# Optimization experiments

Hardware: AMD Instinct MI355X
Metric: run time of the kernel (lower is better)

The kernel has to match this reference:

```python
import jax, jax.numpy as jnp
import numpy as np

INV_SQRT2 = 0.7071067811865476  # 1/sqrt(2), orthonormal Haar
N_LEVELS = 3


def setup_inputs() -> dict:
    key = jax.random.key(0)
    ks = jax.random.split(key, 5)
    B, S, D = 16, 4096, 512
    x = jax.random.normal(ks[0], (B, S, D), dtype=jnp.float32)
    sizes = [256, 128, 64]  # detail-band sizes for 3-level DWT of 512
    Wd0 = jax.random.normal(ks[1], (sizes[0], sizes[0]), dtype=jnp.float32) * 0.02
    Wd1 = jax.random.normal(ks[2], (sizes[1], sizes[1]), dtype=jnp.float32) * 0.02
    Wd2 = jax.random.normal(ks[3], (sizes[2], sizes[2]), dtype=jnp.float32) * 0.02
    Wa = jax.random.normal(ks[4], (sizes[2], sizes[2]), dtype=jnp.float32) * 0.02
    return {
        'x': x,
        'Wd0': Wd0, 'bd0': jnp.zeros((sizes[0],), jnp.float32),
        'Wd1': Wd1, 'bd1': jnp.zeros((sizes[1],), jnp.float32),
        'Wd2': Wd2, 'bd2': jnp.zeros((sizes[2],), jnp.float32),
        'Wa': Wa, 'ba': jnp.zeros((sizes[2],), jnp.float32),
    }


def reference(x, Wd0, bd0, Wd1, bd1, Wd2, bd2, Wa, ba):
    # Multi-level Haar DWT along the feature axis.
    details = []
    a = x
    for _ in range(N_LEVELS):
        e = a[..., 0::2]
        o = a[..., 1::2]
        details.append((e - o) * INV_SQRT2)  # detail coefficients
        a = (e + o) * INV_SQRT2              # approximation coefficients

    # Per-level small linear transforms (torch Linear: y = x @ W.T + b).
    Wds, bds = [Wd0, Wd1, Wd2], [bd0, bd1, bd2]
    details = [details[i] @ Wds[i].T + bds[i] for i in range(N_LEVELS)]
    a = a @ Wa.T + ba

    # Inverse Haar DWT (orthonormal): even=(a+d)/sqrt2, odd=(a-d)/sqrt2, interleave.
    for i in reversed(range(N_LEVELS)):
        d = details[i]
        e = (a + d) * INV_SQRT2
        o = (a - d) * INV_SQRT2
        a = jnp.stack([e, o], axis=-1).reshape(a.shape[:-1] + (a.shape[-1] * 2,))
    return a
```

## Files before the change

kernel.cpp:

```cpp
#include <hip/hip_runtime.h>
#include <stdint.h>

typedef float  f32x4  __attribute__((ext_vector_type(4)));
typedef short  bf16x8 __attribute__((ext_vector_type(8)));
typedef int    i32x4  __attribute__((ext_vector_type(4)));
typedef unsigned int u32x2 __attribute__((ext_vector_type(2)));

#define C1f 0.70710678118654752f
#define C2f 0.5f
#define C3f 0.35355339059327373f

#define NT 512
#define CH 64
#define RB 1040
#define CHSZ (CH*RB)
#define RPB 256
#define NCHUNK (RPB/CH)
#define NCOLG 4

__device__ __forceinline__ unsigned int f2b(float f) {
    unsigned int u; __builtin_memcpy(&u, &f, 4);
    u += 0x7fffu + ((u >> 16) & 1u);
    return u >> 16;
}
__device__ __forceinline__ unsigned int pack2(float lo, float hi) {
    return f2b(lo) | (f2b(hi) << 16);
}
__device__ __forceinline__ bf16x8 cast8(i32x4 v) {
    bf16x8 r; __builtin_memcpy(&r, &v, 16); return r;
}

__device__ __forceinline__ void lds_barrier() {
    asm volatile("s_waitcnt lgkmcnt(0)" ::: "memory");
    __builtin_amdgcn_s_barrier();
    __builtin_amdgcn_sched_barrier(0);
}
__device__ __forceinline__ void vwait4() {
    asm volatile("s_waitcnt vmcnt(4)" ::: "memory");
    __builtin_amdgcn_sched_barrier(0);
}

__device__ __forceinline__ bf16x8 g_frag(int o, int i0,
        const float* __restrict__ W0, const float* __restrict__ W1,
        const float* __restrict__ W2, const float* __restrict__ Wa)
{
    const float s0o = (o & 1) ? -1.f : 1.f;
    const float s1o = ((o >> 1) & 1) ? -1.f : 1.f;
    const float s2o = ((o >> 2) & 1) ? -1.f : 1.f;
    const float4 w0 = *(const float4*)(W0 + (o >> 1) * 256 + (i0 >> 1));
    const float2 w1 = *(const float2*)(W1 + (o >> 2) * 128 + (i0 >> 2));
    const float  w2 = W2[(o >> 3) * 64 + (i0 >> 3)];
    const float  wa = Wa[(o >> 3) * 64 + (i0 >> 3)];
    const float base = 0.125f * wa;
    const float c2   = 0.125f * s2o * w2;
    const float c1   = 0.25f  * s1o;
    const float c0   = 0.5f   * s0o;
    const float w0a[4] = { w0.x, w0.y, w0.z, w0.w };
    const float w1a[2] = { w1.x, w1.y };
    float g[8];
    #pragma unroll
    for (int e = 0; e < 8; ++e) {
        const float t2 = ((e >> 2) & 1) ? -c2 : c2;
        const float t1 = (((e >> 1) & 1) ? -c1 : c1) * w1a[e >> 2];
        const float t0 = ((e & 1) ? -c0 : c0) * w0a[e >> 1];
        g[e] = base + t2 + t1 + t0;
    }
    i32x4 p = { (int)pack2(g[0],g[1]), (int)pack2(g[2],g[3]),
                (int)pack2(g[4],g[5]), (int)pack2(g[6],g[7]) };
    return cast8(p);
}

__global__ void prep(const float* __restrict__ W0, const float* __restrict__ b0,
                     const float* __restrict__ W1, const float* __restrict__ b1,
                     const float* __restrict__ W2, const float* __restrict__ b2,
                     const float* __restrict__ Wa, const float* __restrict__ ba,
                     unsigned short* __restrict__ ws)
{
    const int gid  = blockIdx.x * 256 + threadIdx.x;
    const int blob = gid >> 6, lane = gid & 63;
    const int otg  = blob >> 4, ks = blob & 15;
    const int o  = otg * 16 + (lane & 15);
    const int i0 = ks * 32 + ((lane >> 4) * 8);
    bf16x8 f = g_frag(o, i0, W0, W1, W2, Wa);
    i32x4 p; __builtin_memcpy(&p, &f, 16);
    *(i32x4*)(ws + blob * 512 + lane * 8) = p;
    if (gid < 512) {
        float* gv = (float*)(ws + 262144);
        const int oo = gid;
        const float s0 = (oo & 1) ? -C1f : C1f;
        const float s1 = ((oo >> 1) & 1) ? -C2f : C2f;
        const float s2 = ((oo >> 2) & 1) ? -C3f : C3f;
        gv[oo] = C3f * ba[oo >> 3] + s2 * b2[oo >> 3] + s1 * b1[oo >> 2] + s0 * b0[oo >> 1];
    }
}

template<int USE_WS>
__global__ __launch_bounds__(NT, 2)
void wavelet_gemm(const float* __restrict__ x,
                  const float* __restrict__ W0, const float* __restrict__ b0,
                  const float* __restrict__ W1, const float* __restrict__ b1,
                  const float* __restrict__ W2, const float* __restrict__ b2,
                  const float* __restrict__ Wa, const float* __restrict__ ba,
                  const unsigned short* __restrict__ wsb,
                  float* __restrict__ out, int nblk)
{
    __shared__ char lds[2 * CHSZ];

    const int tid  = threadIdx.x;
    const int lane = tid & 63;
    const int wave = tid >> 6;

    const int cpx = nblk >> 3;
    const int lbid = ((int)blockIdx.x & 7) * cpx + ((int)blockIdx.x >> 3);
    const int colg = lbid & (NCOLG - 1);
    const long rowblk = (long)(lbid >> 2) * RPB;

    const int otg  = colg * 8 + wave;
    const int col0 = otg * 16;
    const int bc0  = col0 + ((lane >> 4) << 2);

    bf16x8 B[16];
    if (USE_WS) {
        #pragma unroll
        for (int ks = 0; ks < 16; ++ks)
            B[ks] = cast8(*(const i32x4*)(wsb + ((size_t)(otg * 16 + ks) * 512) + lane * 8));
    } else {
        #pragma unroll
        for (int ks = 0; ks < 16; ++ks)
            B[ks] = g_frag(col0 + (lane & 15), ks * 32 + ((lane >> 4) * 8), W0, W1, W2, Wa);
    }
    #pragma unroll
    for (int ks = 0; ks < 16; ++ks) {
        i32x4 t; __builtin_memcpy(&t, &B[ks], 16);
        asm volatile("" : "+v"(t));
        __builtin_memcpy(&B[ks], &t, 16);
    }

    f32x4 gv4;
    if (USE_WS) {
        const float4 g4 = *(const float4*)((const float*)(wsb + 262144) + bc0);
        gv4 = f32x4{ g4.x, g4.y, g4.z, g4.w };
    } else {
        #pragma unroll
        for (int j = 0; j < 4; ++j) {
            const int col = bc0 + j;
            const float s0 = (col & 1) ? -C1f : C1f;
            const float s1 = ((col >> 1) & 1) ? -C2f : C2f;
            const float s2 = ((col >> 2) & 1) ? -C3f : C3f;
            gv4[j] = C3f * ba[col >> 3] + s2 * b2[col >> 3] + s1 * b1[col >> 2] + s0 * b0[col >> 1];
        }
    }

    auto ldx = [&](int c, f32x4* v) {
        const f32x4* xb = (const f32x4*)(x + (rowblk + (long)c * CH) * 512);
        #pragma unroll
        for (int i = 0; i < 16; ++i) v[i] = xb[i * NT + tid];
    };
    auto stx = [&](int c, const f32x4* v) {
        char* base = lds + (c & 1) * CHSZ;
        #pragma unroll
        for (int i = 0; i < 16; ++i) {
            const int f = i * NT + tid;
            const int row = f >> 7, c4 = f & 127;
            u32x2 p = { pack2(v[i][0], v[i][1]), pack2(v[i][2], v[i][3]) };
            *(u32x2*)(base + row * RB + c4 * 8) = p;
        }
    };
    auto compute = [&](int c) {
        const char* base = lds + (c & 1) * CHSZ + (lane & 15) * RB + ((lane >> 4) * 16);
        const long r0 = rowblk + (long)c * CH + (lane & 15);
        #pragma unroll
        for (int m = 0; m < 4; ++m) {
            const char* pa = base + m * 16 * RB;
            f32x4 acc = {};
            #pragma unroll
            for (int ks = 0; ks < 16; ++ks) {
                bf16x8 a = cast8(*(const i32x4*)(pa + ks * 64));
                acc = __builtin_amdgcn_mfma_f32_16x16x32_bf16(B[ks], a, acc, 0, 0, 0);
            }
            *(f32x4*)(out + (r0 + m * 16) * 512 + bc0) = acc + gv4;
        }
    };

    {
        f32x4 v[16];
        ldx(0, v);
        stx(0, v);
    }
    lds_barrier();

    #pragma unroll 1
    for (int c = 0; c < NCHUNK; ++c) {
        f32x4 vn[16];
        if (c + 1 < NCHUNK) {
            ldx(c + 1, vn);
            __builtin_amdgcn_sched_barrier(0);
        }
        compute(c);
        if (c + 1 < NCHUNK) {
            vwait4();
            stx(c + 1, vn);
            lds_barrier();
        }
    }
}

extern "C" void kernel_launch(void* const* d_in, const int* in_sizes, int n_in,
                              void* d_out, int out_size, void* d_ws, size_t ws_size,
                              hipStream_t stream)
{
    const float* x  = (const float*)d_in[0];
    const float* W0 = (const float*)d_in[1];
    const float* b0 = (const float*)d_in[2];
    const float* W1 = (const float*)d_in[3];
    const float* b1 = (const float*)d_in[4];
    const float* W2 = (const float*)d_in[5];
    const float* b2 = (const float*)d_in[6];
    const float* Wa = (const float*)d_in[7];
    const float* ba = (const float*)d_in[8];
    float* out = (float*)d_out;

    const int nrows = in_sizes[0] / 512;
    const int nblk  = (nrows / RPB) * NCOLG;

    if (ws_size >= (size_t)(524288 + 2048)) {
        unsigned short* ws = (unsigned short*)d_ws;
        prep<<<128, 256, 0, stream>>>(W0, b0, W1, b1, W2, b2, Wa, ba, ws);
        wavelet_gemm<1><<<nblk, NT, 0, stream>>>(x, W0, b0, W1, b1, W2, b2, Wa, ba, ws, out, nblk);
    } else {
        wavelet_gemm<0><<<nblk, NT, 0, stream>>>(x, W0, b0, W1, b1, W2, b2, Wa, ba, nullptr, out, nblk);
    }
}
```

Baseline: 88.13 us.

## Give each wave two output column tiles and halve row chunk size

```diff
diff --git a/kernel.cpp b/kernel.cpp
--- a/kernel.cpp
+++ b/kernel.cpp
@@ -11,12 +11,11 @@
 #define C3f 0.35355339059327373f
 
 #define NT 512
-#define CH 64
+#define CH 32
 #define RB 1040
 #define CHSZ (CH*RB)
 #define RPB 256
 #define NCHUNK (RPB/CH)
-#define NCOLG 4
 
 __device__ __forceinline__ unsigned int f2b(float f) {
     unsigned int u; __builtin_memcpy(&u, &f, 4);
@@ -112,54 +111,67 @@
 
     const int cpx = nblk >> 3;
     const int lbid = ((int)blockIdx.x & 7) * cpx + ((int)blockIdx.x >> 3);
-    const int colg = lbid & (NCOLG - 1);
-    const long rowblk = (long)(lbid >> 2) * RPB;
-
-    const int otg  = colg * 8 + wave;
-    const int col0 = otg * 16;
+    const int chalf = lbid & 1;
+    const long rowblk = (long)(lbid >> 1) * RPB;
+
+    const int otg0 = chalf * 16 + wave * 2;
+    const int col0 = otg0 * 16;
     const int bc0  = col0 + ((lane >> 4) << 2);
 
-    bf16x8 B[16];
+    bf16x8 B0[16], B1[16];
     if (USE_WS) {
         #pragma unroll
-        for (int ks = 0; ks < 16; ++ks)
-            B[ks] = cast8(*(const i32x4*)(wsb + ((size_t)(otg * 16 + ks) * 512) + lane * 8));
+        for (int ks = 0; ks < 16; ++ks) {
+            B0[ks] = cast8(*(const i32x4*)(wsb + ((size_t)(otg0 * 16 + ks) * 512) + lane * 8));
+            B1[ks] = cast8(*(const i32x4*)(wsb + ((size_t)((otg0 + 1) * 16 + ks) * 512) + lane * 8));
+        }
     } else {
         #pragma unroll
-        for (int ks = 0; ks < 16; ++ks)
-            B[ks] = g_frag(col0 + (lane & 15), ks * 32 + ((lane >> 4) * 8), W0, W1, W2, Wa);
+        for (int ks = 0; ks < 16; ++ks) {
+            B0[ks] = g_frag(col0 + (lane & 15),      ks * 32 + ((lane >> 4) * 8), W0, W1, W2, Wa);
+            B1[ks] = g_frag(col0 + 16 + (lane & 15), ks * 32 + ((lane >> 4) * 8), W0, W1, W2, Wa);
+        }
     }
     #pragma unroll
     for (int ks = 0; ks < 16; ++ks) {
-        i32x4 t; __builtin_memcpy(&t, &B[ks], 16);
-        asm volatile("" : "+v"(t));
-        __builtin_memcpy(&B[ks], &t, 16);
-    }
-
-    f32x4 gv4;
+        i32x4 t0, t1;
+        __builtin_memcpy(&t0, &B0[ks], 16);
+        __builtin_memcpy(&t1, &B1[ks], 16);
+        asm volatile("" : "+v"(t0), "+v"(t1));
+        __builtin_memcpy(&B0[ks], &t0, 16);
+        __builtin_memcpy(&B1[ks], &t1, 16);
+    }
+
+    f32x4 gv40, gv41;
     if (USE_WS) {
-        const float4 g4 = *(const float4*)((const float*)(wsb + 262144) + bc0);
-        gv4 = f32x4{ g4.x, g4.y, g4.z, g4.w };
+        const float4 g0 = *(const float4*)((const float*)(wsb + 262144) + bc0);
+        const float4 g1 = *(const float4*)((const float*)(wsb + 262144) + bc0 + 16);
+        gv40 = f32x4{ g0.x, g0.y, g0.z, g0.w };
+        gv41 = f32x4{ g1.x, g1.y, g1.z, g1.w };
     } else {
         #pragma unroll
         for (int j = 0; j < 4; ++j) {
-            const int col = bc0 + j;
-            const float s0 = (col & 1) ? -C1f : C1f;
-            const float s1 = ((col >> 1) & 1) ? -C2f : C2f;
-            const float s2 = ((col >> 2) & 1) ? -C3f : C3f;
-            gv4[j] = C3f * ba[col >> 3] + s2 * b2[col >> 3] + s1 * b1[col >> 2] + s0 * b0[col >> 1];
+            #pragma unroll
+            for (int t = 0; t < 2; ++t) {
+                const int col = bc0 + t * 16 + j;
+                const float s0 = (col & 1) ? -C1f : C1f;
+                const float s1 = ((col >> 1) & 1) ? -C2f : C2f;
+                const float s2 = ((col >> 2) & 1) ? -C3f : C3f;
+                const float v = C3f * ba[col >> 3] + s2 * b2[col >> 3] + s1 * b1[col >> 2] + s0 * b0[col >> 1];
+                if (t == 0) gv40[j] = v; else gv41[j] = v;
+            }
         }
     }
 
     auto ldx = [&](int c, f32x4* v) {
         const f32x4* xb = (const f32x4*)(x + (rowblk + (long)c * CH) * 512);
         #pragma unroll
-        for (int i = 0; i < 16; ++i) v[i] = xb[i * NT + tid];
+        for (int i = 0; i < 8; ++i) v[i] = xb[i * NT + tid];
     };
     auto stx = [&](int c, const f32x4* v) {
         char* base = lds + (c & 1) * CHSZ;
         #pragma unroll
-        for (int i = 0; i < 16; ++i) {
+        for (int i = 0; i < 8; ++i) {
             const int f = i * NT + tid;
             const int row = f >> 7, c4 = f & 127;
             u32x2 p = { pack2(v[i][0], v[i][1]), pack2(v[i][2], v[i][3]) };
@@ -170,20 +182,23 @@
         const char* base = lds + (c & 1) * CHSZ + (lane & 15) * RB + ((lane >> 4) * 16);
         const long r0 = rowblk + (long)c * CH + (lane & 15);
         #pragma unroll
-        for (int m = 0; m < 4; ++m) {
+        for (int m = 0; m < 2; ++m) {
             const char* pa = base + m * 16 * RB;
-            f32x4 acc = {};
+            f32x4 acc0 = {}, acc1 = {};
             #pragma unroll
             for (int ks = 0; ks < 16; ++ks) {
                 bf16x8 a = cast8(*(const i32x4*)(pa + ks * 64));
-                acc = __builtin_amdgcn_mfma_f32_16x16x32_bf16(B[ks], a, acc, 0, 0, 0);
+                acc0 = __builtin_amdgcn_mfma_f32_16x16x32_bf16(B0[ks], a, acc0, 0, 0, 0);
+                acc1 = __builtin_amdgcn_mfma_f32_16x16x32_bf16(B1[ks], a, acc1, 0, 0, 0);
             }
-            *(f32x4*)(out + (r0 + m * 16) * 512 + bc0) = acc + gv4;
+            const long rr = (r0 + m * 16) * 512;
+            *(f32x4*)(out + rr + bc0)      = acc0 + gv40;
+            *(f32x4*)(out + rr + bc0 + 16) = acc1 + gv41;
         }
     };
 
     {
-        f32x4 v[16];
+        f32x4 v[8];
         ldx(0, v);
         stx(0, v);
     }
@@ -191,7 +206,7 @@
 
     #pragma unroll 1
     for (int c = 0; c < NCHUNK; ++c) {
-        f32x4 vn[16];
+        f32x4 vn[8];
         if (c + 1 < NCHUNK) {
             ldx(c + 1, vn);
             __builtin_amdgcn_sched_barrier(0);
@@ -200,8 +215,8 @@
         if (c + 1 < NCHUNK) {
             vwait4();
             stx(c + 1, vn);
-            lds_barrier();
-        }
+        }
+        lds_barrier();
     }
 }
 
@@ -221,7 +236,7 @@
     float* out = (float*)d_out;
 
     const int nrows = in_sizes[0] / 512;
-    const int nblk  = (nrows / RPB) * NCOLG;
+    const int nblk  = (nrows / RPB) * 2;
 
     if (ws_size >= (size_t)(524288 + 2048)) {
         unsigned short* ws = (unsigned short*)d_ws;
```

After: 75.72 us. -14.1%, faster.
